# Optimization experiments

Hardware: AMD Instinct MI355X
Metric: run time of the kernel (lower is better)

Reference implementation:

```python
import jax, jax.numpy as jnp
import numpy as np

DIM = 256
BETA = 4
B, L, L1 = 16, 2048, 4096
EPS = 1e-6


def setup_inputs() -> dict:
    key = jax.random.key(0)
    ks = jax.random.split(key, 20)
    d, db = DIM, DIM // BETA
    s = lambda *sh: 0.02
    inp = {
        "features": jax.random.normal(ks[0], (B, L, d), jnp.float32),
        "quires_box": jax.random.uniform(ks[1], (B, L1, 2), jnp.float32),
        "quires_features": jax.random.normal(ks[2], (B, L1, d), jnp.float32),
        "pos_feature": jax.random.normal(ks[3], (B, L1, d), jnp.float32),
        # contrast1 params
        "c1_w1": jax.random.normal(ks[4], (db, d), jnp.float32) * 0.02,
        "c1_b1": jnp.zeros((db,), jnp.float32),
        "c1_w2": jax.random.normal(ks[5], (d, db), jnp.float32) * 0.02,
        "c1_b2": jnp.zeros((d,), jnp.float32),
        "c1_g": jnp.ones((d,), jnp.float32),
        "c1_be": jnp.zeros((d,), jnp.float32),
        # contrast2 params
        "c2_w1": jax.random.normal(ks[6], (db, d), jnp.float32) * 0.02,
        "c2_b1": jnp.zeros((db,), jnp.float32),
        "c2_w2": jax.random.normal(ks[7], (d, db), jnp.float32) * 0.02,
        "c2_b2": jnp.zeros((d,), jnp.float32),
        "c2_g": jnp.ones((d,), jnp.float32),
        "c2_be": jnp.zeros((d,), jnp.float32),
        # gate MLP (Prediction: Linear(2d->d)+ReLU+Linear(d->2), dropout=identity at eval)
        "g_w1": jax.random.normal(ks[8], (d, 2 * d), jnp.float32) * 0.02,
        "g_b1": jnp.zeros((d,), jnp.float32),
        "g_w2": jax.random.normal(ks[9], (2, d), jnp.float32) * 0.02,
        "g_b2": jnp.zeros((2,), jnp.float32),
    }
    return inp


def _contrast(v1, v2, w1, b1, w2, b2, g, be):
    # v1, v2: [B, N, C]. Pointwise conv1 -> ReLU -> conv2 -> LayerNorm -> sigmoid -> *v1
    v = v1 * v2
    h = jax.nn.relu(jnp.einsum('bnc,dc->bnd', v, w1) + b1)  # [B,N,C/beta]
    u = jnp.einsum('bnd,cd->bnc', h, w2) + b2               # [B,N,C]
    mu = jnp.mean(u, axis=-1, keepdims=True)
    var = jnp.mean(jnp.square(u - mu), axis=-1, keepdims=True)
    ln = (u - mu) * jax.lax.rsqrt(var + EPS) * g + be
    return jax.nn.sigmoid(ln) * v1


def reference(features, quires_box, quires_features, pos_feature,
              c1_w1, c1_b1, c1_w2, c1_b2, c1_g, c1_be,
              c2_w1, c2_b1, c2_w2, c2_b2, c2_g, c2_be,
              g_w1, g_b1, g_w2, g_b2):
    Lf = features.shape[1]
    cx, w = quires_box[..., 0], quires_box[..., 1]
    roi_start = jnp.round(jnp.clip((cx - w / 2) * Lf, 0, Lf - 1)).astype(jnp.int32)
    roi_end = jnp.round(jnp.clip((cx + w / 2) * Lf, 0, Lf - 1)).astype(jnp.int32)
    sf = jnp.take_along_axis(features, roi_start[..., None], axis=1)  # [B,L1,C]
    ef = jnp.take_along_axis(features, roi_end[..., None], axis=1)    # [B,L1,C]
    sf = _contrast(sf, pos_feature, c1_w1, c1_b1, c1_w2, c1_b2, c1_g, c1_be)
    ef = _contrast(ef, pos_feature, c2_w1, c2_b1, c2_w2, c2_b2, c2_g, c2_be)
    pooled = (sf + ef) * 0.5  # aligned_len=True -> mean over the 2 boundaries
    x = jnp.concatenate([pooled, quires_features], axis=-1)  # [B,L1,2C]
    h = jax.nn.relu(jnp.einsum('bnc,dc->bnd', x, g_w1) + g_b1)
    gate = jax.nn.softmax(jnp.einsum('bnd,od->bno', h, g_w2) + g_b2, axis=-1)
    out = pooled * gate[..., 0:1] + quires_features * gate[..., 1:2]
    return jnp.swapaxes(out, 0, 1)  # [L1, B, C]
```

## Files before the change

### kernel.cpp

```cpp
#include <hip/hip_runtime.h>
#include <hip/hip_bf16.h>
#include <math.h>

typedef __attribute__((ext_vector_type(8))) short bf16x8;
typedef __attribute__((ext_vector_type(4))) float f32x4;
typedef __attribute__((ext_vector_type(2))) __fp16 f16x2;
typedef __attribute__((ext_vector_type(4))) unsigned int u32x4;
typedef __attribute__((ext_vector_type(2))) unsigned int u32x2;

constexpr int NB = 16, NQ = 4096, LF = 2048, C = 256;

__device__ __forceinline__ unsigned short bfbits(float x) {
    return __builtin_bit_cast(unsigned short, __float2bfloat16(x));
}
__device__ __forceinline__ unsigned pk2(float a, float b) {
    return (unsigned)bfbits(a) | ((unsigned)bfbits(b) << 16);
}
__device__ __forceinline__ float bflo(unsigned d) { return __builtin_bit_cast(float, d << 16); }
__device__ __forceinline__ float bfhi(unsigned d) { return __builtin_bit_cast(float, d & 0xffff0000u); }
__device__ __forceinline__ unsigned pkh(float a, float b) {
    f16x2 h = __builtin_amdgcn_cvt_pkrtz(a, b);
    return __builtin_bit_cast(unsigned, h);
}
__device__ __forceinline__ float hlo(unsigned u) {
    f16x2 h = __builtin_bit_cast(f16x2, u); return (float)h[0];
}
__device__ __forceinline__ float hhi(unsigned u) {
    f16x2 h = __builtin_bit_cast(f16x2, u); return (float)h[1];
}

__global__ void prep_weights(const float* __restrict__ c1w1, const float* __restrict__ c2w1,
                             const float* __restrict__ c1w2, const float* __restrict__ c2w2,
                             const float* __restrict__ gw1, unsigned short* __restrict__ ws)
{
    int t = blockIdx.x * 256 + threadIdx.x;
    const float* src; int K, nks, dstoff, f;
    if (t < 2048)      { src = c1w1; K = 256; nks = 8;  dstoff = 0;      f = t; }
    else if (t < 4096) { src = c2w1; K = 256; nks = 8;  dstoff = 16384;  f = t - 2048; }
    else if (t < 6144) { src = c1w2; K = 64;  nks = 2;  dstoff = 32768;  f = t - 4096; }
    else if (t < 8192) { src = c2w2; K = 64;  nks = 2;  dstoff = 49152;  f = t - 6144; }
    else               { src = gw1;  K = 512; nks = 16; dstoff = 65536;  f = t - 8192; }
    int l = f & 63, s = f >> 6;
    int nt = s / nks, ks = s % nks;
    int n  = nt * 16 + (l & 15);
    int k0 = ks * 32 + (l >> 4) * 8;
    unsigned short* d = ws + dstoff + (size_t)f * 8;
    const float* sp = src + (size_t)n * K + k0;
    #pragma unroll
    for (int e = 0; e < 8; ++e) d[e] = bfbits(sp[e]);
}

__global__ __launch_bounds__(256, 4)
void semalign_v14(const float* __restrict__ feat,  const float* __restrict__ qbox,
                  const float* __restrict__ qfeat, const float* __restrict__ posf,
                  const float* __restrict__ c1b1,  const float* __restrict__ c1b2,
                  const float* __restrict__ c1g,   const float* __restrict__ c1be,
                  const float* __restrict__ c2b1,  const float* __restrict__ c2b2,
                  const float* __restrict__ c2g,   const float* __restrict__ c2be,
                  const float* __restrict__ gb1,   const float* __restrict__ gw2,
                  const float* __restrict__ gb2,
                  const unsigned short* __restrict__ wsb,
                  float* __restrict__ out)
{
    __shared__ __align__(16) unsigned short sP[4][16][256];

    const int tid = threadIdx.x, l = tid & 63, wid = tid >> 6;
    const int lr = l & 15, lg = l >> 4;
    const int rowb = blockIdx.x * 64 + wid * 16;
    const int q = rowb >> 4;
    const int b = lr;
    const int swz = (lr & 7) << 4;

    const float* prow = posf  + ((size_t)b * NQ + q) * C;
    const float* qrow = qfeat + ((size_t)b * NQ + q) * C;
    float cx = qbox[((size_t)b * NQ + q) * 2 + 0];
    float w  = qbox[((size_t)b * NQ + q) * 2 + 1];
    float fs = fminf(fmaxf((cx - 0.5f * w) * (float)LF, 0.f), (float)(LF - 1));
    float fe = fminf(fmaxf((cx + 0.5f * w) * (float)LF, 0.f), (float)(LF - 1));
    const float* srow = feat + ((size_t)b * LF + (int)rintf(fs)) * C;
    const float* erow = feat + ((size_t)b * LF + (int)rintf(fe)) * C;

    bf16x8 v1f[8], v2f[8];
    #pragma unroll
    for (int ks = 0; ks < 8; ++ks) {
        int k0 = ks * 32 + lg * 8;
        float4 s0 = *(const float4*)(srow + k0), s1 = *(const float4*)(srow + k0 + 4);
        float4 e0 = *(const float4*)(erow + k0), e1 = *(const float4*)(erow + k0 + 4);
        float4 p0 = *(const float4*)(prow + k0), p1 = *(const float4*)(prow + k0 + 4);
        u32x4 a, c;
        a[0] = pk2(s0.x * p0.x, s0.y * p0.y); a[1] = pk2(s0.z * p0.z, s0.w * p0.w);
        a[2] = pk2(s1.x * p1.x, s1.y * p1.y); a[3] = pk2(s1.z * p1.z, s1.w * p1.w);
        c[0] = pk2(e0.x * p0.x, e0.y * p0.y); c[1] = pk2(e0.z * p0.z, e0.w * p0.w);
        c[2] = pk2(e1.x * p1.x, e1.y * p1.y); c[3] = pk2(e1.z * p1.z, e1.w * p1.w);
        v1f[ks] = __builtin_bit_cast(bf16x8, a);
        v2f[ks] = __builtin_bit_cast(bf16x8, c);
    }

    char* pb = (char*)&sP[wid][0][0];
    {
        f32x4 a1[4] = {}, a2[4] = {};
        #pragma unroll
        for (int ks = 0; ks < 8; ++ks) {
            #pragma unroll
            for (int nt = 0; nt < 4; ++nt) {
                bf16x8 wA = *(const bf16x8*)(wsb + ((size_t)((nt * 8 + ks) * 64 + l)) * 8);
                bf16x8 wB = *(const bf16x8*)(wsb + 16384 + ((size_t)((nt * 8 + ks) * 64 + l)) * 8);
                a1[nt] = __builtin_amdgcn_mfma_f32_16x16x32_bf16(wA, v1f[ks], a1[nt], 0, 0, 0);
                a2[nt] = __builtin_amdgcn_mfma_f32_16x16x32_bf16(wB, v2f[ks], a2[nt], 0, 0, 0);
            }
        }
        #pragma unroll
        for (int nt = 0; nt < 4; ++nt) {
            float4 b1v = *(const float4*)(c1b1 + nt * 16 + lg * 4);
            float4 b2v = *(const float4*)(c2b1 + nt * 16 + lg * 4);
            u32x2 wv;
            wv[0] = pk2(fmaxf(a1[nt][0] + b1v.x, 0.f), fmaxf(a1[nt][1] + b1v.y, 0.f));
            wv[1] = pk2(fmaxf(a1[nt][2] + b1v.z, 0.f), fmaxf(a1[nt][3] + b1v.w, 0.f));
            *(u32x2*)(pb + lr * 128 + ((nt * 32 + lg * 8) ^ swz)) = wv;
            wv[0] = pk2(fmaxf(a2[nt][0] + b2v.x, 0.f), fmaxf(a2[nt][1] + b2v.y, 0.f));
            wv[1] = pk2(fmaxf(a2[nt][2] + b2v.z, 0.f), fmaxf(a2[nt][3] + b2v.w, 0.f));
            *(u32x2*)(pb + 2048 + lr * 128 + ((nt * 32 + lg * 8) ^ swz)) = wv;
        }
    }

    f16x2 Ph[16][2];
    #pragma unroll
    for (int j = 0; j < 2; ++j) {
        char* hb = pb + j * 2048;
        asm volatile("s_waitcnt lgkmcnt(0)" ::: "memory");
        bf16x8 hf0 = *(const bf16x8*)(hb + lr * 128 + ((0 + lg * 16) ^ swz));
        bf16x8 hf1 = *(const bf16x8*)(hb + lr * 128 + ((64 + lg * 16) ^ swz));
        const unsigned short* w2b = wsb + (j ? 49152 : 32768);
        const float* b2p = j ? c2b2 : c1b2;
        const float* gp  = j ? c2g  : c1g;
        const float* bep = j ? c2be : c1be;
        const float* xrow = j ? erow : srow;
        float S = 0.f, Q2 = 0.f;

        {
            f32x4 u8[8] = {};
            #pragma unroll
            for (int nt = 0; nt < 8; ++nt) {
                bf16x8 wA = *(const bf16x8*)(w2b + ((size_t)((nt * 2 + 0) * 64 + l)) * 8);
                bf16x8 wB = *(const bf16x8*)(w2b + ((size_t)((nt * 2 + 1) * 64 + l)) * 8);
                u8[nt] = __builtin_amdgcn_mfma_f32_16x16x32_bf16(wA, hf0, u8[nt], 0, 0, 0);
                u8[nt] = __builtin_amdgcn_mfma_f32_16x16x32_bf16(wB, hf1, u8[nt], 0, 0, 0);
            }
            #pragma unroll
            for (int nt = 0; nt < 8; ++nt) {
                float4 bv = *(const float4*)(b2p + nt * 16 + lg * 4);
                u8[nt][0] += bv.x; u8[nt][1] += bv.y; u8[nt][2] += bv.z; u8[nt][3] += bv.w;
                S  += u8[nt][0] + u8[nt][1] + u8[nt][2] + u8[nt][3];
                Q2 += u8[nt][0] * u8[nt][0] + u8[nt][1] * u8[nt][1]
                    + u8[nt][2] * u8[nt][2] + u8[nt][3] * u8[nt][3];
                u32x2 wv;
                wv[0] = pkh(u8[nt][0], u8[nt][1]);
                wv[1] = pkh(u8[nt][2], u8[nt][3]);
                *(u32x2*)(pb + 4096 + nt * 512 + l * 8) = wv;
            }
        }
        f32x4 u8b[8] = {};
        #pragma unroll
        for (int nt = 0; nt < 8; ++nt) {
            bf16x8 wA = *(const bf16x8*)(w2b + ((size_t)(((nt + 8) * 2 + 0) * 64 + l)) * 8);
            bf16x8 wB = *(const bf16x8*)(w2b + ((size_t)(((nt + 8) * 2 + 1) * 64 + l)) * 8);
            u8b[nt] = __builtin_amdgcn_mfma_f32_16x16x32_bf16(wA, hf0, u8b[nt], 0, 0, 0);
            u8b[nt] = __builtin_amdgcn_mfma_f32_16x16x32_bf16(wB, hf1, u8b[nt], 0, 0, 0);
        }
        #pragma unroll
        for (int nt = 0; nt < 8; ++nt) {
            float4 bv = *(const float4*)(b2p + (nt + 8) * 16 + lg * 4);
            u8b[nt][0] += bv.x; u8b[nt][1] += bv.y; u8b[nt][2] += bv.z; u8b[nt][3] += bv.w;
            S  += u8b[nt][0] + u8b[nt][1] + u8b[nt][2] + u8b[nt][3];
            Q2 += u8b[nt][0] * u8b[nt][0] + u8b[nt][1] * u8b[nt][1]
                + u8b[nt][2] * u8b[nt][2] + u8b[nt][3] * u8b[nt][3];
        }
        S  += __shfl_xor(S, 16);  S  += __shfl_xor(S, 32);
        Q2 += __shfl_xor(Q2, 16); Q2 += __shfl_xor(Q2, 32);
        float mu  = S * (1.f / 256.f);
        float rsg = rsqrtf(Q2 * (1.f / 256.f) - mu * mu + 1e-6f);

        u32x2 st[8];
        asm volatile("s_waitcnt lgkmcnt(0)" ::: "memory");
        #pragma unroll
        for (int nt = 0; nt < 8; ++nt)
            st[nt] = *(const u32x2*)(pb + 4096 + nt * 512 + l * 8);
        asm volatile("s_waitcnt lgkmcnt(0)" ::: "memory");

        #pragma unroll
        for (int nt = 0; nt < 16; ++nt) {
            float u4[4];
            if (nt < 8) {
                u4[0] = hlo(st[nt][0]); u4[1] = hhi(st[nt][0]);
                u4[2] = hlo(st[nt][1]); u4[3] = hhi(st[nt][1]);
            } else {
                u4[0] = u8b[nt - 8][0]; u4[1] = u8b[nt - 8][1];
                u4[2] = u8b[nt - 8][2]; u4[3] = u8b[nt - 8][3];
            }
            float4 gv  = *(const float4*)(gp  + nt * 16 + lg * 4);
            float4 bev = *(const float4*)(bep + nt * 16 + lg * 4);
            float4 xv  = *(const float4*)(xrow + nt * 16 + lg * 4);
            float g4[4] = { gv.x, gv.y, gv.z, gv.w };
            float e4[4] = { bev.x, bev.y, bev.z, bev.w };
            float x4[4] = { xv.x, xv.y, xv.z, xv.w };
            float tm[4];
            #pragma unroll
            for (int r = 0; r < 4; ++r) {
                float ln = (u4[r] - mu) * rsg * g4[r] + e4[r];
                float sg = 1.f / (1.f + __expf(-ln));
                tm[r] = 0.5f * sg * x4[r];
            }
            if (j == 0) {
                Ph[nt][0] = __builtin_amdgcn_cvt_pkrtz(tm[0], tm[1]);
                Ph[nt][1] = __builtin_amdgcn_cvt_pkrtz(tm[2], tm[3]);
            } else {
                float p0 = (float)Ph[nt][0][0] + tm[0];
                float p1 = (float)Ph[nt][0][1] + tm[1];
                float p2 = (float)Ph[nt][1][0] + tm[2];
                float p3 = (float)Ph[nt][1][1] + tm[3];
                u32x2 wv;
                wv[0] = pk2(p0, p1); wv[1] = pk2(p2, p3);
                *(u32x2*)(pb + lr * 512 + ((nt * 32 + lg * 8) ^ swz)) = wv;
            }
        }
    }
    asm volatile("s_waitcnt lgkmcnt(0)" ::: "memory");

    f32x4 ga[16] = {};
    const unsigned short* gwb = wsb + 65536;
    #pragma clang loop unroll(disable)
    for (int kk = 0; kk < 16; ++kk) {
        bf16x8 xk;
        if (kk < 8) {
            xk = *(const bf16x8*)(pb + lr * 512 + ((kk * 64 + lg * 16) ^ swz));
        } else {
            int k0 = (kk - 8) * 32 + lg * 8;
            float4 q0 = *(const float4*)(qrow + k0), q1 = *(const float4*)(qrow + k0 + 4);
            u32x4 a;
            a[0] = pk2(q0.x, q0.y); a[1] = pk2(q0.z, q0.w);
            a[2] = pk2(q1.x, q1.y); a[3] = pk2(q1.z, q1.w);
            xk = __builtin_bit_cast(bf16x8, a);
        }
        #pragma unroll
        for (int nt = 0; nt < 16; ++nt) {
            bf16x8 wf = *(const bf16x8*)(gwb + ((size_t)((nt * 16 + kk) * 64 + l)) * 8);
            ga[nt] = __builtin_amdgcn_mfma_f32_16x16x32_bf16(wf, xk, ga[nt], 0, 0, 0);
        }
    }

    float t0 = 0.f, t1 = 0.f;
    #pragma unroll
    for (int nt = 0; nt < 16; ++nt) {
        float4 gbv = *(const float4*)(gb1 + nt * 16 + lg * 4);
        float4 w0v = *(const float4*)(gw2 + nt * 16 + lg * 4);
        float4 w1v = *(const float4*)(gw2 + 256 + nt * 16 + lg * 4);
        float gb4[4] = { gbv.x, gbv.y, gbv.z, gbv.w };
        float w04[4] = { w0v.x, w0v.y, w0v.z, w0v.w };
        float w14[4] = { w1v.x, w1v.y, w1v.z, w1v.w };
        #pragma unroll
        for (int r = 0; r < 4; ++r) {
            float hv = fmaxf(ga[nt][r] + gb4[r], 0.f);
            t0 += hv * w04[r]; t1 += hv * w14[r];
        }
    }
    t0 += __shfl_xor(t0, 16); t0 += __shfl_xor(t0, 32);
    t1 += __shfl_xor(t1, 16); t1 += __shfl_xor(t1, 32);
    float g0 = 1.f / (1.f + __expf((t1 + gb2[1]) - (t0 + gb2[0])));
    float g1 = 1.f - g0;

    float* orow = out + (size_t)(rowb + lr) * C;
    #pragma unroll
    for (int ks = 0; ks < 8; ++ks) {
        bf16x8 pf = *(const bf16x8*)(pb + lr * 512 + ((ks * 64 + lg * 16) ^ swz));
        u32x4 pu = __builtin_bit_cast(u32x4, pf);
        int k0 = ks * 32 + lg * 8;
        float4 q0 = *(const float4*)(qrow + k0), q1 = *(const float4*)(qrow + k0 + 4);
        float4 o0, o1;
        o0.x = bflo(pu[0]) * g0 + q0.x * g1;
        o0.y = bfhi(pu[0]) * g0 + q0.y * g1;
        o0.z = bflo(pu[1]) * g0 + q0.z * g1;
        o0.w = bfhi(pu[1]) * g0 + q0.w * g1;
        o1.x = bflo(pu[2]) * g0 + q1.x * g1;
        o1.y = bfhi(pu[2]) * g0 + q1.y * g1;
        o1.z = bflo(pu[3]) * g0 + q1.z * g1;
        o1.w = bfhi(pu[3]) * g0 + q1.w * g1;
        *(float4*)(orow + ks * 32 + lg * 8)     = o0;
        *(float4*)(orow + ks * 32 + lg * 8 + 4) = o1;
    }
}

extern "C" void kernel_launch(void* const* d_in, const int* in_sizes, int n_in,
                              void* d_out, int out_size, void* d_ws, size_t ws_size,
                              hipStream_t stream) {
    const float* feat  = (const float*)d_in[0];
    const float* qbox  = (const float*)d_in[1];
    const float* qfeat = (const float*)d_in[2];
    const float* posf  = (const float*)d_in[3];
    const float* c1w1  = (const float*)d_in[4];
    const float* c1b1  = (const float*)d_in[5];
    const float* c1w2  = (const float*)d_in[6];
    const float* c1b2  = (const float*)d_in[7];
    const float* c1g   = (const float*)d_in[8];
    const float* c1be  = (const float*)d_in[9];
    const float* c2w1  = (const float*)d_in[10];
    const float* c2b1  = (const float*)d_in[11];
    const float* c2w2  = (const float*)d_in[12];
    const float* c2b2  = (const float*)d_in[13];
    const float* c2g   = (const float*)d_in[14];
    const float* c2be  = (const float*)d_in[15];
    const float* gw1   = (const float*)d_in[16];
    const float* gb1   = (const float*)d_in[17];
    const float* gw2   = (const float*)d_in[18];
    const float* gb2   = (const float*)d_in[19];
    float* out = (float*)d_out;
    unsigned short* wsb = (unsigned short*)d_ws;

    prep_weights<<<96, 256, 0, stream>>>(c1w1, c2w1, c1w2, c2w2, gw1, wsb);

    dim3 grid((NB * NQ) / 64), block(256);
    semalign_v14<<<grid, block, 0, stream>>>(
        feat, qbox, qfeat, posf,
        c1b1, c1b2, c1g, c1be,
        c2b1, c2b2, c2g, c2be,
        gb1, gw2, gb2, wsb, out);
}
```

Measured before the change: 164.1 us.

## Switch to 32x32x16 MFMA tiles with 32 rows per wave

Moves every matmul from 16x16x32 to 32x32x16 bf16 MFMA, so each wave handles 32 query rows and blocks shrink to two waves of 128 threads. The weight prepack layout is changed to match the new fragment shape. The first contrast layer is fused into the gather loop, and the second layer's output is recomputed in a second pass instead of being staged in fp16 through shared memory. The gate matmul is split into four passes so fewer accumulators are live at once. Larger tiles mean fewer weight-fragment loads per row, at the cost of extra MFMA work for the recompute and possibly more registers per thread.

New measurement: 318.7 us. 1.94x slower.

```diff
diff --git a/kernel.cpp b/kernel.cpp
--- a/kernel.cpp
+++ b/kernel.cpp
@@ -3,8 +3,7 @@
 #include <math.h>
 
 typedef __attribute__((ext_vector_type(8))) short bf16x8;
-typedef __attribute__((ext_vector_type(4))) float f32x4;
-typedef __attribute__((ext_vector_type(2))) __fp16 f16x2;
+typedef __attribute__((ext_vector_type(16))) float f32x16;
 typedef __attribute__((ext_vector_type(4))) unsigned int u32x4;
 typedef __attribute__((ext_vector_type(2))) unsigned int u32x2;
 
@@ -18,16 +17,6 @@
 }
 __device__ __forceinline__ float bflo(unsigned d) { return __builtin_bit_cast(float, d << 16); }
 __device__ __forceinline__ float bfhi(unsigned d) { return __builtin_bit_cast(float, d & 0xffff0000u); }
-__device__ __forceinline__ unsigned pkh(float a, float b) {
-    f16x2 h = __builtin_amdgcn_cvt_pkrtz(a, b);
-    return __builtin_bit_cast(unsigned, h);
-}
-__device__ __forceinline__ float hlo(unsigned u) {
-    f16x2 h = __builtin_bit_cast(f16x2, u); return (float)h[0];
-}
-__device__ __forceinline__ float hhi(unsigned u) {
-    f16x2 h = __builtin_bit_cast(f16x2, u); return (float)h[1];
-}
 
 __global__ void prep_weights(const float* __restrict__ c1w1, const float* __restrict__ c2w1,
                              const float* __restrict__ c1w2, const float* __restrict__ c2w2,
@@ -35,23 +24,23 @@
 {
     int t = blockIdx.x * 256 + threadIdx.x;
     const float* src; int K, nks, dstoff, f;
-    if (t < 2048)      { src = c1w1; K = 256; nks = 8;  dstoff = 0;      f = t; }
-    else if (t < 4096) { src = c2w1; K = 256; nks = 8;  dstoff = 16384;  f = t - 2048; }
-    else if (t < 6144) { src = c1w2; K = 64;  nks = 2;  dstoff = 32768;  f = t - 4096; }
-    else if (t < 8192) { src = c2w2; K = 64;  nks = 2;  dstoff = 49152;  f = t - 6144; }
-    else               { src = gw1;  K = 512; nks = 16; dstoff = 65536;  f = t - 8192; }
+    if (t < 2048)      { src = c1w1; K = 256; nks = 16; dstoff = 0;      f = t; }
+    else if (t < 4096) { src = c2w1; K = 256; nks = 16; dstoff = 16384;  f = t - 2048; }
+    else if (t < 6144) { src = c1w2; K = 64;  nks = 4;  dstoff = 32768;  f = t - 4096; }
+    else if (t < 8192) { src = c2w2; K = 64;  nks = 4;  dstoff = 49152;  f = t - 6144; }
+    else               { src = gw1;  K = 512; nks = 32; dstoff = 65536;  f = t - 8192; }
     int l = f & 63, s = f >> 6;
     int nt = s / nks, ks = s % nks;
-    int n  = nt * 16 + (l & 15);
-    int k0 = ks * 32 + (l >> 4) * 8;
+    int n  = nt * 32 + (l & 31);
+    int k0 = ks * 16 + (l >> 5) * 8;
     unsigned short* d = ws + dstoff + (size_t)f * 8;
     const float* sp = src + (size_t)n * K + k0;
     #pragma unroll
     for (int e = 0; e < 8; ++e) d[e] = bfbits(sp[e]);
 }
 
-__global__ __launch_bounds__(256, 4)
-void semalign_v14(const float* __restrict__ feat,  const float* __restrict__ qbox,
+__global__ __launch_bounds__(128, 4)
+void semalign_v16(const float* __restrict__ feat,  const float* __restrict__ qbox,
                   const float* __restrict__ qfeat, const float* __restrict__ posf,
                   const float* __restrict__ c1b1,  const float* __restrict__ c1b2,
                   const float* __restrict__ c1g,   const float* __restrict__ c1be,
@@ -62,14 +51,15 @@
                   const unsigned short* __restrict__ wsb,
                   float* __restrict__ out)
 {
-    __shared__ __align__(16) unsigned short sP[4][16][256];
+    __shared__ __align__(16) unsigned short sR[2][32][256];
 
     const int tid = threadIdx.x, l = tid & 63, wid = tid >> 6;
-    const int lr = l & 15, lg = l >> 4;
-    const int rowb = blockIdx.x * 64 + wid * 16;
-    const int q = rowb >> 4;
-    const int b = lr;
-    const int swz = (lr & 7) << 4;
+    const int c = l & 31, kh = l >> 5;
+    const int rowb = blockIdx.x * 64 + wid * 32;
+    const int b = c & 15;
+    const int q = (rowb >> 4) + (c >> 4);
+    const int swz = (c & 7) << 4;
+    char* pbase = (char*)&sR[wid][0][0];
 
     const float* prow = posf  + ((size_t)b * NQ + q) * C;
     const float* qrow = qfeat + ((size_t)b * NQ + q) * C;
@@ -80,201 +70,198 @@
     const float* srow = feat + ((size_t)b * LF + (int)rintf(fs)) * C;
     const float* erow = feat + ((size_t)b * LF + (int)rintf(fe)) * C;
 
-    bf16x8 v1f[8], v2f[8];
-    #pragma unroll
-    for (int ks = 0; ks < 8; ++ks) {
-        int k0 = ks * 32 + lg * 8;
-        float4 s0 = *(const float4*)(srow + k0), s1 = *(const float4*)(srow + k0 + 4);
-        float4 e0 = *(const float4*)(erow + k0), e1 = *(const float4*)(erow + k0 + 4);
-        float4 p0 = *(const float4*)(prow + k0), p1 = *(const float4*)(prow + k0 + 4);
-        u32x4 a, c;
-        a[0] = pk2(s0.x * p0.x, s0.y * p0.y); a[1] = pk2(s0.z * p0.z, s0.w * p0.w);
-        a[2] = pk2(s1.x * p1.x, s1.y * p1.y); a[3] = pk2(s1.z * p1.z, s1.w * p1.w);
-        c[0] = pk2(e0.x * p0.x, e0.y * p0.y); c[1] = pk2(e0.z * p0.z, e0.w * p0.w);
-        c[2] = pk2(e1.x * p1.x, e1.y * p1.y); c[3] = pk2(e1.z * p1.z, e1.w * p1.w);
-        v1f[ks] = __builtin_bit_cast(bf16x8, a);
-        v2f[ks] = __builtin_bit_cast(bf16x8, c);
-    }
-
-    char* pb = (char*)&sP[wid][0][0];
-    {
-        f32x4 a1[4] = {}, a2[4] = {};
-        #pragma unroll
-        for (int ks = 0; ks < 8; ++ks) {
-            #pragma unroll
-            for (int nt = 0; nt < 4; ++nt) {
-                bf16x8 wA = *(const bf16x8*)(wsb + ((size_t)((nt * 8 + ks) * 64 + l)) * 8);
-                bf16x8 wB = *(const bf16x8*)(wsb + 16384 + ((size_t)((nt * 8 + ks) * 64 + l)) * 8);
-                a1[nt] = __builtin_amdgcn_mfma_f32_16x16x32_bf16(wA, v1f[ks], a1[nt], 0, 0, 0);
-                a2[nt] = __builtin_amdgcn_mfma_f32_16x16x32_bf16(wB, v2f[ks], a2[nt], 0, 0, 0);
-            }
-        }
-        #pragma unroll
-        for (int nt = 0; nt < 4; ++nt) {
-            float4 b1v = *(const float4*)(c1b1 + nt * 16 + lg * 4);
-            float4 b2v = *(const float4*)(c2b1 + nt * 16 + lg * 4);
-            u32x2 wv;
-            wv[0] = pk2(fmaxf(a1[nt][0] + b1v.x, 0.f), fmaxf(a1[nt][1] + b1v.y, 0.f));
-            wv[1] = pk2(fmaxf(a1[nt][2] + b1v.z, 0.f), fmaxf(a1[nt][3] + b1v.w, 0.f));
-            *(u32x2*)(pb + lr * 128 + ((nt * 32 + lg * 8) ^ swz)) = wv;
-            wv[0] = pk2(fmaxf(a2[nt][0] + b2v.x, 0.f), fmaxf(a2[nt][1] + b2v.y, 0.f));
-            wv[1] = pk2(fmaxf(a2[nt][2] + b2v.z, 0.f), fmaxf(a2[nt][3] + b2v.w, 0.f));
-            *(u32x2*)(pb + 2048 + lr * 128 + ((nt * 32 + lg * 8) ^ swz)) = wv;
-        }
-    }
-
-    f16x2 Ph[16][2];
+    bf16x8 hf1[4], hf2[4];
     #pragma unroll
     for (int j = 0; j < 2; ++j) {
-        char* hb = pb + j * 2048;
+        const unsigned short* w1b = wsb + (j ? 16384 : 0);
+        const float* xr  = j ? erow : srow;
+        const float* b1p = j ? c2b1 : c1b1;
+        f32x16 a0 = {}, a1 = {};
+        #pragma unroll
+        for (int ks = 0; ks < 16; ++ks) {
+            int k0 = ks * 16 + kh * 8;
+            float4 x0 = *(const float4*)(xr + k0),  x1 = *(const float4*)(xr + k0 + 4);
+            float4 p0 = *(const float4*)(prow + k0), p1 = *(const float4*)(prow + k0 + 4);
+            u32x4 a;
+            a[0] = pk2(x0.x * p0.x, x0.y * p0.y); a[1] = pk2(x0.z * p0.z, x0.w * p0.w);
+            a[2] = pk2(x1.x * p1.x, x1.y * p1.y); a[3] = pk2(x1.z * p1.z, x1.w * p1.w);
+            bf16x8 v = __builtin_bit_cast(bf16x8, a);
+            bf16x8 w0 = *(const bf16x8*)(w1b + ((size_t)((0 * 16 + ks) * 64 + l)) * 8);
+            bf16x8 w1f = *(const bf16x8*)(w1b + ((size_t)((1 * 16 + ks) * 64 + l)) * 8);
+            a0 = __builtin_amdgcn_mfma_f32_32x32x16_bf16(w0, v, a0, 0, 0, 0);
+            a1 = __builtin_amdgcn_mfma_f32_32x32x16_bf16(w1f, v, a1, 0, 0, 0);
+        }
+        #pragma unroll
+        for (int nt = 0; nt < 2; ++nt) {
+            f32x16 acc = nt ? a1 : a0;
+            #pragma unroll
+            for (int g = 0; g < 4; ++g) {
+                int n0 = nt * 32 + 8 * g + 4 * kh;
+                float4 bv = *(const float4*)(b1p + n0);
+                u32x2 wv;
+                wv[0] = pk2(fmaxf(acc[4 * g + 0] + bv.x, 0.f), fmaxf(acc[4 * g + 1] + bv.y, 0.f));
+                wv[1] = pk2(fmaxf(acc[4 * g + 2] + bv.z, 0.f), fmaxf(acc[4 * g + 3] + bv.w, 0.f));
+                *(u32x2*)(pbase + c * 128 + ((n0 * 2) ^ swz)) = wv;
+            }
+        }
         asm volatile("s_waitcnt lgkmcnt(0)" ::: "memory");
-        bf16x8 hf0 = *(const bf16x8*)(hb + lr * 128 + ((0 + lg * 16) ^ swz));
-        bf16x8 hf1 = *(const bf16x8*)(hb + lr * 128 + ((64 + lg * 16) ^ swz));
+        #pragma unroll
+        for (int ks2 = 0; ks2 < 4; ++ks2) {
+            bf16x8 h = *(const bf16x8*)(pbase + c * 128 + (((ks2 * 16 + kh * 8) * 2) ^ swz));
+            if (j == 0) hf1[ks2] = h; else hf2[ks2] = h;
+        }
+        asm volatile("s_waitcnt lgkmcnt(0)" ::: "memory");
+    }
+
+    float S1 = 0.f, Q21 = 0.f, S2 = 0.f, Q22 = 0.f;
+    #pragma unroll
+    for (int j = 0; j < 2; ++j) {
         const unsigned short* w2b = wsb + (j ? 49152 : 32768);
         const float* b2p = j ? c2b2 : c1b2;
-        const float* gp  = j ? c2g  : c1g;
-        const float* bep = j ? c2be : c1be;
-        const float* xrow = j ? erow : srow;
         float S = 0.f, Q2 = 0.f;
-
+        #pragma unroll
+        for (int nt = 0; nt < 8; ++nt) {
+            f32x16 u = {};
+            #pragma unroll
+            for (int ks2 = 0; ks2 < 4; ++ks2) {
+                bf16x8 wf = *(const bf16x8*)(w2b + ((size_t)((nt * 4 + ks2) * 64 + l)) * 8);
+                u = __builtin_amdgcn_mfma_f32_32x32x16_bf16(wf, j ? hf2[ks2] : hf1[ks2], u, 0, 0, 0);
+            }
+            #pragma unroll
+            for (int g = 0; g < 4; ++g) {
+                int n0 = nt * 32 + 8 * g + 4 * kh;
+                float4 bv = *(const float4*)(b2p + n0);
+                float b4[4] = { bv.x, bv.y, bv.z, bv.w };
+                #pragma unroll
+                for (int r = 0; r < 4; ++r) {
+                    float v = u[4 * g + r] + b4[r];
+                    S += v; Q2 += v * v;
+                }
+            }
+        }
+        if (j == 0) { S1 = S; Q21 = Q2; } else { S2 = S; Q22 = Q2; }
+    }
+    S1 += __shfl_xor(S1, 32); Q21 += __shfl_xor(Q21, 32);
+    S2 += __shfl_xor(S2, 32); Q22 += __shfl_xor(Q22, 32);
+    float mu1 = S1 * (1.f / 256.f), rs1 = rsqrtf(Q21 * (1.f / 256.f) - mu1 * mu1 + 1e-6f);
+    float mu2 = S2 * (1.f / 256.f), rs2 = rsqrtf(Q22 * (1.f / 256.f) - mu2 * mu2 + 1e-6f);
+
+    #pragma unroll
+    for (int nt = 0; nt < 8; ++nt) {
+        float tm1[16];
         {
-            f32x4 u8[8] = {};
-            #pragma unroll
-            for (int nt = 0; nt < 8; ++nt) {
-                bf16x8 wA = *(const bf16x8*)(w2b + ((size_t)((nt * 2 + 0) * 64 + l)) * 8);
-                bf16x8 wB = *(const bf16x8*)(w2b + ((size_t)((nt * 2 + 1) * 64 + l)) * 8);
-                u8[nt] = __builtin_amdgcn_mfma_f32_16x16x32_bf16(wA, hf0, u8[nt], 0, 0, 0);
-                u8[nt] = __builtin_amdgcn_mfma_f32_16x16x32_bf16(wB, hf1, u8[nt], 0, 0, 0);
-            }
-            #pragma unroll
-            for (int nt = 0; nt < 8; ++nt) {
-                float4 bv = *(const float4*)(b2p + nt * 16 + lg * 4);
-                u8[nt][0] += bv.x; u8[nt][1] += bv.y; u8[nt][2] += bv.z; u8[nt][3] += bv.w;
-                S  += u8[nt][0] + u8[nt][1] + u8[nt][2] + u8[nt][3];
-                Q2 += u8[nt][0] * u8[nt][0] + u8[nt][1] * u8[nt][1]
-                    + u8[nt][2] * u8[nt][2] + u8[nt][3] * u8[nt][3];
+            f32x16 u = {};
+            #pragma unroll
+            for (int ks2 = 0; ks2 < 4; ++ks2) {
+                bf16x8 wf = *(const bf16x8*)(wsb + 32768 + ((size_t)((nt * 4 + ks2) * 64 + l)) * 8);
+                u = __builtin_amdgcn_mfma_f32_32x32x16_bf16(wf, hf1[ks2], u, 0, 0, 0);
+            }
+            #pragma unroll
+            for (int g = 0; g < 4; ++g) {
+                int n0 = nt * 32 + 8 * g + 4 * kh;
+                float4 bv = *(const float4*)(c1b2 + n0);
+                float4 gv = *(const float4*)(c1g  + n0);
+                float4 ev = *(const float4*)(c1be + n0);
+                float4 xv = *(const float4*)(srow + n0);
+                float b4[4] = { bv.x, bv.y, bv.z, bv.w };
+                float g4[4] = { gv.x, gv.y, gv.z, gv.w };
+                float e4[4] = { ev.x, ev.y, ev.z, ev.w };
+                float x4[4] = { xv.x, xv.y, xv.z, xv.w };
+                #pragma unroll
+                for (int r = 0; r < 4; ++r) {
+                    float ln = (u[4 * g + r] + b4[r] - mu1) * rs1 * g4[r] + e4[r];
+                    float sg = 1.f / (1.f + __expf(-ln));
+                    tm1[4 * g + r] = 0.5f * sg * x4[r];
+                }
+            }
+        }
+        {
+            f32x16 u = {};
+            #pragma unroll
+            for (int ks2 = 0; ks2 < 4; ++ks2) {
+                bf16x8 wf = *(const bf16x8*)(wsb + 49152 + ((size_t)((nt * 4 + ks2) * 64 + l)) * 8);
+                u = __builtin_amdgcn_mfma_f32_32x32x16_bf16(wf, hf2[ks2], u, 0, 0, 0);
+            }
+            #pragma unroll
+            for (int g = 0; g < 4; ++g) {
+                int n0 = nt * 32 + 8 * g + 4 * kh;
+                float4 bv = *(const float4*)(c2b2 + n0);
+                float4 gv = *(const float4*)(c2g  + n0);
+                float4 ev = *(const float4*)(c2be + n0);
+                float4 xv = *(const float4*)(erow + n0);
+                float b4[4] = { bv.x, bv.y, bv.z, bv.w };
+                float g4[4] = { gv.x, gv.y, gv.z, gv.w };
+                float e4[4] = { ev.x, ev.y, ev.z, ev.w };
+                float x4[4] = { xv.x, xv.y, xv.z, xv.w };
+                float pm[4];
+                #pragma unroll
+                for (int r = 0; r < 4; ++r) {
+                    float ln = (u[4 * g + r] + b4[r] - mu2) * rs2 * g4[r] + e4[r];
+                    float sg = 1.f / (1.f + __expf(-ln));
+                    pm[r] = tm1[4 * g + r] + 0.5f * sg * x4[r];
+                }
                 u32x2 wv;
-                wv[0] = pkh(u8[nt][0], u8[nt][1]);
-                wv[1] = pkh(u8[nt][2], u8[nt][3]);
-                *(u32x2*)(pb + 4096 + nt * 512 + l * 8) = wv;
-            }
-        }
-        f32x4 u8b[8] = {};
-        #pragma unroll
-        for (int nt = 0; nt < 8; ++nt) {
-            bf16x8 wA = *(const bf16x8*)(w2b + ((size_t)(((nt + 8) * 2 + 0) * 64 + l)) * 8);
-            bf16x8 wB = *(const bf16x8*)(w2b + ((size_t)(((nt + 8) * 2 + 1) * 64 + l)) * 8);
-            u8b[nt] = __builtin_amdgcn_mfma_f32_16x16x32_bf16(wA, hf0, u8b[nt], 0, 0, 0);
-            u8b[nt] = __builtin_amdgcn_mfma_f32_16x16x32_bf16(wB, hf1, u8b[nt], 0, 0, 0);
-        }
-        #pragma unroll
-        for (int nt = 0; nt < 8; ++nt) {
-            float4 bv = *(const float4*)(b2p + (nt + 8) * 16 + lg * 4);
-            u8b[nt][0] += bv.x; u8b[nt][1] += bv.y; u8b[nt][2] += bv.z; u8b[nt][3] += bv.w;
-            S  += u8b[nt][0] + u8b[nt][1] + u8b[nt][2] + u8b[nt][3];
-            Q2 += u8b[nt][0] * u8b[nt][0] + u8b[nt][1] * u8b[nt][1]
-                + u8b[nt][2] * u8b[nt][2] + u8b[nt][3] * u8b[nt][3];
-        }
-        S  += __shfl_xor(S, 16);  S  += __shfl_xor(S, 32);
-        Q2 += __shfl_xor(Q2, 16); Q2 += __shfl_xor(Q2, 32);
-        float mu  = S * (1.f / 256.f);
-        float rsg = rsqrtf(Q2 * (1.f / 256.f) - mu * mu + 1e-6f);
-
-        u32x2 st[8];
-        asm volatile("s_waitcnt lgkmcnt(0)" ::: "memory");
-        #pragma unroll
-        for (int nt = 0; nt < 8; ++nt)
-            st[nt] = *(const u32x2*)(pb + 4096 + nt * 512 + l * 8);
-        asm volatile("s_waitcnt lgkmcnt(0)" ::: "memory");
-
-        #pragma unroll
-        for (int nt = 0; nt < 16; ++nt) {
-            float u4[4];
-            if (nt < 8) {
-                u4[0] = hlo(st[nt][0]); u4[1] = hhi(st[nt][0]);
-                u4[2] = hlo(st[nt][1]); u4[3] = hhi(st[nt][1]);
-            } else {
-                u4[0] = u8b[nt - 8][0]; u4[1] = u8b[nt - 8][1];
-                u4[2] = u8b[nt - 8][2]; u4[3] = u8b[nt - 8][3];
-            }
-            float4 gv  = *(const float4*)(gp  + nt * 16 + lg * 4);
-            float4 bev = *(const float4*)(bep + nt * 16 + lg * 4);
-            float4 xv  = *(const float4*)(xrow + nt * 16 + lg * 4);
-            float g4[4] = { gv.x, gv.y, gv.z, gv.w };
-            float e4[4] = { bev.x, bev.y, bev.z, bev.w };
-            float x4[4] = { xv.x, xv.y, xv.z, xv.w };
-            float tm[4];
-            #pragma unroll
-            for (int r = 0; r < 4; ++r) {
-                float ln = (u4[r] - mu) * rsg * g4[r] + e4[r];
-                float sg = 1.f / (1.f + __expf(-ln));
-                tm[r] = 0.5f * sg * x4[r];
-            }
-            if (j == 0) {
-                Ph[nt][0] = __builtin_amdgcn_cvt_pkrtz(tm[0], tm[1]);
-                Ph[nt][1] = __builtin_amdgcn_cvt_pkrtz(tm[2], tm[3]);
-            } else {
-                float p0 = (float)Ph[nt][0][0] + tm[0];
-                float p1 = (float)Ph[nt][0][1] + tm[1];
-                float p2 = (float)Ph[nt][1][0] + tm[2];
-                float p3 = (float)Ph[nt][1][1] + tm[3];
-                u32x2 wv;
-                wv[0] = pk2(p0, p1); wv[1] = pk2(p2, p3);
-                *(u32x2*)(pb + lr * 512 + ((nt * 32 + lg * 8) ^ swz)) = wv;
+                wv[0] = pk2(pm[0], pm[1]); wv[1] = pk2(pm[2], pm[3]);
+                *(u32x2*)(pbase + c * 512 + ((nt * 64 + 16 * g + 8 * kh) ^ swz)) = wv;
             }
         }
     }
     asm volatile("s_waitcnt lgkmcnt(0)" ::: "memory");
 
-    f32x4 ga[16] = {};
+    float t0 = 0.f, t1 = 0.f;
     const unsigned short* gwb = wsb + 65536;
     #pragma clang loop unroll(disable)
-    for (int kk = 0; kk < 16; ++kk) {
-        bf16x8 xk;
-        if (kk < 8) {
-            xk = *(const bf16x8*)(pb + lr * 512 + ((kk * 64 + lg * 16) ^ swz));
-        } else {
-            int k0 = (kk - 8) * 32 + lg * 8;
-            float4 q0 = *(const float4*)(qrow + k0), q1 = *(const float4*)(qrow + k0 + 4);
-            u32x4 a;
-            a[0] = pk2(q0.x, q0.y); a[1] = pk2(q0.z, q0.w);
-            a[2] = pk2(q1.x, q1.y); a[3] = pk2(q1.z, q1.w);
-            xk = __builtin_bit_cast(bf16x8, a);
-        }
-        #pragma unroll
-        for (int nt = 0; nt < 16; ++nt) {
-            bf16x8 wf = *(const bf16x8*)(gwb + ((size_t)((nt * 16 + kk) * 64 + l)) * 8);
-            ga[nt] = __builtin_amdgcn_mfma_f32_16x16x32_bf16(wf, xk, ga[nt], 0, 0, 0);
-        }
-    }
-
-    float t0 = 0.f, t1 = 0.f;
-    #pragma unroll
-    for (int nt = 0; nt < 16; ++nt) {
-        float4 gbv = *(const float4*)(gb1 + nt * 16 + lg * 4);
-        float4 w0v = *(const float4*)(gw2 + nt * 16 + lg * 4);
-        float4 w1v = *(const float4*)(gw2 + 256 + nt * 16 + lg * 4);
-        float gb4[4] = { gbv.x, gbv.y, gbv.z, gbv.w };
-        float w04[4] = { w0v.x, w0v.y, w0v.z, w0v.w };
-        float w14[4] = { w1v.x, w1v.y, w1v.z, w1v.w };
-        #pragma unroll
-        for (int r = 0; r < 4; ++r) {
-            float hv = fmaxf(ga[nt][r] + gb4[r], 0.f);
-            t0 += hv * w04[r]; t1 += hv * w14[r];
-        }
-    }
-    t0 += __shfl_xor(t0, 16); t0 += __shfl_xor(t0, 32);
-    t1 += __shfl_xor(t1, 16); t1 += __shfl_xor(t1, 32);
+    for (int p = 0; p < 4; ++p) {
+        f32x16 ga0 = {}, ga1 = {};
+        #pragma clang loop unroll(disable)
+        for (int kk = 0; kk < 32; ++kk) {
+            bf16x8 xk;
+            if (kk < 16) {
+                xk = *(const bf16x8*)(pbase + c * 512 + (((kk * 16 + kh * 8) * 2) ^ swz));
+            } else {
+                int k0 = (kk - 16) * 16 + kh * 8;
+                float4 q0 = *(const float4*)(qrow + k0), q1 = *(const float4*)(qrow + k0 + 4);
+                u32x4 a;
+                a[0] = pk2(q0.x, q0.y); a[1] = pk2(q0.z, q0.w);
+                a[2] = pk2(q1.x, q1.y); a[3] = pk2(q1.z, q1.w);
+                xk = __builtin_bit_cast(bf16x8, a);
+            }
+            bf16x8 w0 = *(const bf16x8*)(gwb + ((size_t)(((2 * p + 0) * 32 + kk) * 64 + l)) * 8);
+            bf16x8 w1f = *(const bf16x8*)(gwb + ((size_t)(((2 * p + 1) * 32 + kk) * 64 + l)) * 8);
+            ga0 = __builtin_amdgcn_mfma_f32_32x32x16_bf16(w0, xk, ga0, 0, 0, 0);
+            ga1 = __builtin_amdgcn_mfma_f32_32x32x16_bf16(w1f, xk, ga1, 0, 0, 0);
+        }
+        #pragma unroll
+        for (int t2 = 0; t2 < 2; ++t2) {
+            f32x16 ga = t2 ? ga1 : ga0;
+            #pragma unroll
+            for (int g = 0; g < 4; ++g) {
+                int n0 = (2 * p + t2) * 32 + 8 * g + 4 * kh;
+                float4 gbv = *(const float4*)(gb1 + n0);
+                float4 w0v = *(const float4*)(gw2 + n0);
+                float4 w1v = *(const float4*)(gw2 + 256 + n0);
+                float gb4[4] = { gbv.x, gbv.y, gbv.z, gbv.w };
+                float w04[4] = { w0v.x, w0v.y, w0v.z, w0v.w };
+                float w14[4] = { w1v.x, w1v.y, w1v.z, w1v.w };
+                #pragma unroll
+                for (int r = 0; r < 4; ++r) {
+                    float hv = fmaxf(ga[4 * g + r] + gb4[r], 0.f);
+                    t0 += hv * w04[r]; t1 += hv * w14[r];
+                }
+            }
+        }
+    }
+    t0 += __shfl_xor(t0, 32); t1 += __shfl_xor(t1, 32);
     float g0 = 1.f / (1.f + __expf((t1 + gb2[1]) - (t0 + gb2[0])));
     float g1 = 1.f - g0;
 
-    float* orow = out + (size_t)(rowb + lr) * C;
-    #pragma unroll
-    for (int ks = 0; ks < 8; ++ks) {
-        bf16x8 pf = *(const bf16x8*)(pb + lr * 512 + ((ks * 64 + lg * 16) ^ swz));
+    float* orow = out + (size_t)(rowb + c) * C;
+    #pragma unroll
+    for (int jj = 0; jj < 16; ++jj) {
+        int ch = kh * 128 + jj * 8;
+        bf16x8 pf = *(const bf16x8*)(pbase + c * 512 + ((ch * 2) ^ swz));
         u32x4 pu = __builtin_bit_cast(u32x4, pf);
-        int k0 = ks * 32 + lg * 8;
-        float4 q0 = *(const float4*)(qrow + k0), q1 = *(const float4*)(qrow + k0 + 4);
+        float4 q0 = *(const float4*)(qrow + ch), q1 = *(const float4*)(qrow + ch + 4);
         float4 o0, o1;
         o0.x = bflo(pu[0]) * g0 + q0.x * g1;
         o0.y = bfhi(pu[0]) * g0 + q0.y * g1;
@@ -284,8 +271,8 @@
         o1.y = bfhi(pu[2]) * g0 + q1.y * g1;
         o1.z = bflo(pu[3]) * g0 + q1.z * g1;
         o1.w = bfhi(pu[3]) * g0 + q1.w * g1;
-        *(float4*)(orow + ks * 32 + lg * 8)     = o0;
-        *(float4*)(orow + ks * 32 + lg * 8 + 4) = o1;
+        *(float4*)(orow + ch)     = o0;
+        *(float4*)(orow + ch + 4) = o1;
     }
 }
 
@@ -317,8 +304,8 @@
 
     prep_weights<<<96, 256, 0, stream>>>(c1w1, c2w1, c1w2, c2w2, gw1, wsb);
 
-    dim3 grid((NB * NQ) / 64), block(256);
-    semalign_v14<<<grid, block, 0, stream>>>(
+    dim3 grid((NB * NQ) / 64), block(128);
+    semalign_v16<<<grid, block, 0, stream>>>(
         feat, qbox, qfeat, posf,
         c1b1, c1b2, c1g, c1be,
         c2b1, c2b2, c2g, c2be,
```
